# Kernel optimization log

Measured on AMD Instinct MI355X. Metric: run time of the kernel, lower is better.

The kernel has to match this reference:

```python
import jax, jax.numpy as jnp
import numpy as np


def setup_inputs() -> dict:
    key = jax.random.key(0)
    k1, k2, k3, k4 = jax.random.split(key, 4)
    B, S, H, U, C = 64, 512, 768, 16, 5
    hidden = jax.random.normal(k1, (B, S, H), dtype=jnp.float32)
    # per-token utterance index, sorted so each utterance is a contiguous span
    segment_ids = jnp.sort(jax.random.randint(k2, (B, S), 0, U), axis=-1).astype(jnp.int32)
    W_h = jax.random.normal(k3, (H, H), dtype=jnp.float32) * 0.02
    b_h = jnp.zeros((H,), dtype=jnp.float32)
    W_o = jax.random.normal(k4, (H, C), dtype=jnp.float32) * 0.02
    b_o = jnp.zeros((C,), dtype=jnp.float32)
    return {"hidden": hidden, "segment_ids": segment_ids, "n_utter": U,
            "W_h": W_h, "b_h": b_h, "W_o": W_o, "b_o": b_o}


def reference(hidden, segment_ids, n_utter, W_h, b_h, W_o, b_o):
    # hidden: [B,S,H]; segment_ids: [B,S] in [0, n_utter)
    B, S, H = hidden.shape
    n_segments = B * n_utter
    # globalize segment ids across the batch
    flat_seg = (segment_ids + jnp.arange(B, dtype=segment_ids.dtype)[:, None] * n_utter).reshape(-1)
    flat_h = hidden.reshape(B * S, H)
    # ragged per-utterance mean via one segment reduce (replaces python slice loop)
    sums = jax.ops.segment_sum(flat_h, flat_seg, num_segments=n_segments)
    counts = jax.ops.segment_sum(jnp.ones((B * S,), dtype=hidden.dtype), flat_seg,
                                 num_segments=n_segments)
    means = sums / jnp.maximum(counts, 1.0)[:, None]  # [B*n_utter, H]
    # linear_h -> SELU -> (dropout is identity in eval) -> linear_o -> softmax
    h = jax.nn.selu(means @ W_h + b_h)
    logits = h @ W_o + b_o
    return jax.nn.softmax(logits, axis=1)
```

## Files before the change

### kernel.cpp

```cpp
#include <hip/hip_runtime.h>
#include <math.h>

#define B 64
#define S 512
#define H 768
#define U 16
#define C 5
#define M (B*U)

typedef __attribute__((ext_vector_type(8))) short short8;
typedef __attribute__((ext_vector_type(4))) float floatx4;

__device__ inline unsigned short f2bf(float x) {
    unsigned u = __float_as_uint(x);
    u += 0x7FFFu + ((u >> 16) & 1u);
    return (unsigned short)(u >> 16);
}
__device__ inline float bf2f(unsigned short b) {
    return __uint_as_float((unsigned)b << 16);
}
__device__ inline void acc4(float4& a, const float4& v) {
    a.x += v.x; a.y += v.y; a.z += v.z; a.w += v.w;
}

__global__ __launch_bounds__(192) void prep_kernel(
    const float* __restrict__ hidden, const int* __restrict__ seg,
    const float* __restrict__ Wh,
    unsigned short* __restrict__ means, unsigned short* __restrict__ Bt)
{
    __shared__ float tile[32][33];
    const int t = threadIdx.x;

    if (blockIdx.x < M) {
        const int b = blockIdx.x >> 4;
        const int u = blockIdx.x & 15;
        const int* srow = seg + b * S;

        int lo = 0, hi = S;
        while (lo < hi) { int mid = (lo + hi) >> 1; if (srow[mid] < u) lo = mid + 1; else hi = mid; }
        const int start = lo;
        hi = S;
        while (lo < hi) { int mid = (lo + hi) >> 1; if (srow[mid] < u + 1) lo = mid + 1; else hi = mid; }
        const int end = lo;

        const float4* h4 = (const float4*)(hidden + (size_t)b * S * H) + t;
        const int ldr = H / 4;

        float4 a0 = make_float4(0.f,0.f,0.f,0.f), a1 = a0, a2 = a0, a3 = a0;
        int s = start;
        #pragma unroll 2
        for (; s + 4 <= end; s += 4) {
            float4 v0 = h4[(size_t)(s + 0) * ldr];
            float4 v1 = h4[(size_t)(s + 1) * ldr];
            float4 v2 = h4[(size_t)(s + 2) * ldr];
            float4 v3 = h4[(size_t)(s + 3) * ldr];
            acc4(a0, v0); acc4(a1, v1); acc4(a2, v2); acc4(a3, v3);
        }
        for (; s < end; ++s) acc4(a0, h4[(size_t)s * ldr]);

        acc4(a0, a1); acc4(a2, a3); acc4(a0, a2);
        const float inv = 1.0f / fmaxf((float)(end - start), 1.0f);
        ushort4 o;
        o.x = f2bf(a0.x * inv); o.y = f2bf(a0.y * inv);
        o.z = f2bf(a0.z * inv); o.w = f2bf(a0.w * inv);
        ((ushort4*)(means + (size_t)(b * U + u) * H))[t] = o;
        return;
    }

    const int tb = blockIdx.x - M;
    const int bn = tb % (H / 32);
    const int bk = tb / (H / 32);
    #pragma unroll
    for (int i = 0; i < 6; ++i) {
        int idx = t + 192 * i;
        if (idx < 1024) {
            int r = idx >> 5, c = idx & 31;
            tile[r][c] = Wh[(size_t)(bk * 32 + r) * H + bn * 32 + c];
        }
    }
    __syncthreads();
    #pragma unroll
    for (int i = 0; i < 6; ++i) {
        int idx = t + 192 * i;
        if (idx < 1024) {
            int r = idx >> 5, c = idx & 31;
            Bt[(size_t)(bn * 32 + r) * H + bk * 32 + c] = f2bf(tile[c][r]);
        }
    }
}

__global__ __launch_bounds__(256) void gemm1_mfma_kernel(
    const unsigned short* __restrict__ means, const unsigned short* __restrict__ Bt,
    const float* __restrict__ bh, unsigned short* __restrict__ hout)
{
    const int wid  = threadIdx.x >> 6;
    const int lane = threadIdx.x & 63;
    const int tile = blockIdx.x * 4 + wid;
    const int tm = tile / (H / 32);
    const int tn = tile % (H / 32);
    const int m0 = tm * 32, n0 = tn * 32;

    const int quad = lane >> 4;
    const int l16  = lane & 15;

    const short8* ap0 = (const short8*)(means + (size_t)(m0 + l16) * H);
    const short8* ap1 = (const short8*)(means + (size_t)(m0 + 16 + l16) * H);
    const short8* bp0 = (const short8*)(Bt    + (size_t)(n0 + l16) * H);
    const short8* bp1 = (const short8*)(Bt    + (size_t)(n0 + 16 + l16) * H);

    floatx4 acc00 = {0.f, 0.f, 0.f, 0.f}, acc01 = acc00, acc10 = acc00, acc11 = acc00;
    #pragma unroll 4
    for (int kk = 0; kk < H / 32; ++kk) {
        short8 a0 = ap0[4 * kk + quad];
        short8 a1 = ap1[4 * kk + quad];
        short8 b0 = bp0[4 * kk + quad];
        short8 b1 = bp1[4 * kk + quad];
        acc00 = __builtin_amdgcn_mfma_f32_16x16x32_bf16(a0, b0, acc00, 0, 0, 0);
        acc01 = __builtin_amdgcn_mfma_f32_16x16x32_bf16(a0, b1, acc01, 0, 0, 0);
        acc10 = __builtin_amdgcn_mfma_f32_16x16x32_bf16(a1, b0, acc10, 0, 0, 0);
        acc11 = __builtin_amdgcn_mfma_f32_16x16x32_bf16(a1, b1, acc11, 0, 0, 0);
    }

    const float SC = 1.0507009873554805f, AL = 1.6732632423543772f;
    const float bs0 = bh[n0 + l16], bs1 = bh[n0 + 16 + l16];
    #pragma unroll
    for (int r = 0; r < 4; ++r) {
        unsigned short* row0 = hout + (size_t)(m0 + quad * 4 + r) * H;
        unsigned short* row1 = hout + (size_t)(m0 + 16 + quad * 4 + r) * H;
        float x;
        x = acc00[r] + bs0; row0[n0 + l16]      = f2bf(x > 0.f ? SC * x : SC * AL * (expf(x) - 1.f));
        x = acc01[r] + bs1; row0[n0 + 16 + l16] = f2bf(x > 0.f ? SC * x : SC * AL * (expf(x) - 1.f));
        x = acc10[r] + bs0; row1[n0 + l16]      = f2bf(x > 0.f ? SC * x : SC * AL * (expf(x) - 1.f));
        x = acc11[r] + bs1; row1[n0 + 16 + l16] = f2bf(x > 0.f ? SC * x : SC * AL * (expf(x) - 1.f));
    }
}

__global__ __launch_bounds__(256) void head_kernel(
    const unsigned short* __restrict__ hbuf, const float* __restrict__ Wo,
    const float* __restrict__ bo, float* __restrict__ out)
{
    const int wave = threadIdx.x >> 6;
    const int lane = threadIdx.x & 63;
    const int row  = blockIdx.x * 4 + wave;

    float acc[C] = {};
    #pragma unroll
    for (int j = 0; j < H / 128; ++j) {
        int k = 128 * j + 2 * lane;
        ushort2 hv = *(const ushort2*)(hbuf + (size_t)row * H + k);
        float h0 = bf2f(hv.x), h1 = bf2f(hv.y);
        #pragma unroll
        for (int cc = 0; cc < C; ++cc)
            acc[cc] += h0 * Wo[(size_t)k * C + cc] + h1 * Wo[(size_t)(k + 1) * C + cc];
    }
    #pragma unroll
    for (int off = 32; off >= 1; off >>= 1)
        #pragma unroll
        for (int cc = 0; cc < C; ++cc) acc[cc] += __shfl_down(acc[cc], off);

    if (lane == 0) {
        float l[C], mx = -1e30f;
        #pragma unroll
        for (int cc = 0; cc < C; ++cc) { l[cc] = acc[cc] + bo[cc]; mx = fmaxf(mx, l[cc]); }
        float sum = 0.f;
        #pragma unroll
        for (int cc = 0; cc < C; ++cc) { l[cc] = expf(l[cc] - mx); sum += l[cc]; }
        float r = 1.0f / sum;
        #pragma unroll
        for (int cc = 0; cc < C; ++cc) out[(size_t)row * C + cc] = l[cc] * r;
    }
}

extern "C" void kernel_launch(void* const* d_in, const int* in_sizes, int n_in,
                              void* d_out, int out_size, void* d_ws, size_t ws_size,
                              hipStream_t stream)
{
    const float* hidden = (const float*)d_in[0];
    const int*   seg    = (const int*)d_in[1];
    const float* Wh = (const float*)d_in[3];
    const float* bh = (const float*)d_in[4];
    const float* Wo = (const float*)d_in[5];
    const float* bo = (const float*)d_in[6];
    float* out = (float*)d_out;

    unsigned short* means = (unsigned short*)d_ws;
    unsigned short* Bt    = means + (size_t)M * H;
    unsigned short* hbuf  = Bt + (size_t)H * H;

    prep_kernel<<<M + (H / 32) * (H / 32), 192, 0, stream>>>(hidden, seg, Wh, means, Bt);
    gemm1_mfma_kernel<<<(M / 32) * (H / 32) / 4, 256, 0, stream>>>(means, Bt, bh, hbuf);
    head_kernel<<<M / 4, 256, 0, stream>>>(hbuf, Wo, bo, out);
}
```

Measured before the change: 181.3 us.

## Fuse three kernels into one cooperative kernel with grid-wide syncs

Merges the segment-mean/weight-transpose prep, the MFMA GEMM with SELU, and the softmax head into a single cooperative kernel of M blocks separated by grid.sync calls. The aim is to remove two kernel launch gaps and inter-kernel drain. The cost is that the GEMM now runs at 3 waves per block over fewer active blocks, and the grid syncs add their own overhead. The launch also depends on all 1024 blocks being co-resident.

```diff
diff --git a/kernel.cpp b/kernel.cpp
--- a/kernel.cpp
+++ b/kernel.cpp
@@ -1,5 +1,8 @@
 #include <hip/hip_runtime.h>
+#include <hip/hip_cooperative_groups.h>
 #include <math.h>
+
+namespace cg = cooperative_groups;
 
 #define B 64
 #define S 512
@@ -23,17 +26,21 @@
     a.x += v.x; a.y += v.y; a.z += v.z; a.w += v.w;
 }
 
-__global__ __launch_bounds__(192) void prep_kernel(
+__global__ __launch_bounds__(192, 3) void fused_kernel(
     const float* __restrict__ hidden, const int* __restrict__ seg,
-    const float* __restrict__ Wh,
-    unsigned short* __restrict__ means, unsigned short* __restrict__ Bt)
+    const float* __restrict__ Wh, const float* __restrict__ bh,
+    const float* __restrict__ Wo, const float* __restrict__ bo,
+    unsigned short* __restrict__ means, unsigned short* __restrict__ Bt,
+    unsigned short* __restrict__ hbuf, float* __restrict__ out)
 {
+    cg::grid_group grid = cg::this_grid();
     __shared__ float tile[32][33];
-    const int t = threadIdx.x;
+    const int t  = threadIdx.x;
+    const int bi = blockIdx.x;
 
-    if (blockIdx.x < M) {
-        const int b = blockIdx.x >> 4;
-        const int u = blockIdx.x & 15;
+    {
+        const int b = bi >> 4;
+        const int u = bi & 15;
         const int* srow = seg + b * S;
 
         int lo = 0, hi = S;
@@ -63,111 +70,109 @@
         ushort4 o;
         o.x = f2bf(a0.x * inv); o.y = f2bf(a0.y * inv);
         o.z = f2bf(a0.z * inv); o.w = f2bf(a0.w * inv);
-        ((ushort4*)(means + (size_t)(b * U + u) * H))[t] = o;
-        return;
+        ((ushort4*)(means + (size_t)bi * H))[t] = o;
     }
 
-    const int tb = blockIdx.x - M;
-    const int bn = tb % (H / 32);
-    const int bk = tb / (H / 32);
-    #pragma unroll
-    for (int i = 0; i < 6; ++i) {
-        int idx = t + 192 * i;
-        if (idx < 1024) {
-            int r = idx >> 5, c = idx & 31;
-            tile[r][c] = Wh[(size_t)(bk * 32 + r) * H + bn * 32 + c];
+    if (bi < (H / 32) * (H / 32)) {
+        const int bn = bi % (H / 32);
+        const int bk = bi / (H / 32);
+        #pragma unroll
+        for (int i = 0; i < 6; ++i) {
+            int idx = t + 192 * i;
+            if (idx < 1024) {
+                int r = idx >> 5, c = idx & 31;
+                tile[r][c] = Wh[(size_t)(bk * 32 + r) * H + bn * 32 + c];
+            }
+        }
+        __syncthreads();
+        #pragma unroll
+        for (int i = 0; i < 6; ++i) {
+            int idx = t + 192 * i;
+            if (idx < 1024) {
+                int r = idx >> 5, c = idx & 31;
+                Bt[(size_t)(bn * 32 + r) * H + bk * 32 + c] = f2bf(tile[c][r]);
+            }
         }
     }
-    __syncthreads();
-    #pragma unroll
-    for (int i = 0; i < 6; ++i) {
-        int idx = t + 192 * i;
-        if (idx < 1024) {
-            int r = idx >> 5, c = idx & 31;
-            Bt[(size_t)(bn * 32 + r) * H + bk * 32 + c] = f2bf(tile[c][r]);
+
+    grid.sync();
+
+    const int wid  = t >> 6;
+    const int lane = t & 63;
+
+    if (bi < (M / 32) * (H / 32) / 3) {
+        const int tileId = bi * 3 + wid;
+        const int tm = tileId / (H / 32);
+        const int tn = tileId % (H / 32);
+        const int m0 = tm * 32, n0 = tn * 32;
+
+        const int quad = lane >> 4;
+        const int l16  = lane & 15;
+
+        const short8* ap0 = (const short8*)(means + (size_t)(m0 + l16) * H);
+        const short8* ap1 = (const short8*)(means + (size_t)(m0 + 16 + l16) * H);
+        const short8* bp0 = (const short8*)(Bt    + (size_t)(n0 + l16) * H);
+        const short8* bp1 = (const short8*)(Bt    + (size_t)(n0 + 16 + l16) * H);
+
+        floatx4 acc00 = {0.f, 0.f, 0.f, 0.f}, acc01 = acc00, acc10 = acc00, acc11 = acc00;
+        #pragma unroll 4
+        for (int kk = 0; kk < H / 32; ++kk) {
+            short8 a0 = ap0[4 * kk + quad];
+            short8 a1 = ap1[4 * kk + quad];
+            short8 b0 = bp0[4 * kk + quad];
+            short8 b1 = bp1[4 * kk + quad];
+            acc00 = __builtin_amdgcn_mfma_f32_16x16x32_bf16(a0, b0, acc00, 0, 0, 0);
+            acc01 = __builtin_amdgcn_mfma_f32_16x16x32_bf16(a0, b1, acc01, 0, 0, 0);
+            acc10 = __builtin_amdgcn_mfma_f32_16x16x32_bf16(a1, b0, acc10, 0, 0, 0);
+            acc11 = __builtin_amdgcn_mfma_f32_16x16x32_bf16(a1, b1, acc11, 0, 0, 0);
+        }
+
+        const float SC = 1.0507009873554805f, AL = 1.6732632423543772f;
+        const float bs0 = bh[n0 + l16], bs1 = bh[n0 + 16 + l16];
+        #pragma unroll
+        for (int r = 0; r < 4; ++r) {
+            unsigned short* row0 = hbuf + (size_t)(m0 + quad * 4 + r) * H;
+            unsigned short* row1 = hbuf + (size_t)(m0 + 16 + quad * 4 + r) * H;
+            float x;
+            x = acc00[r] + bs0; row0[n0 + l16]      = f2bf(x > 0.f ? SC * x : SC * AL * (expf(x) - 1.f));
+            x = acc01[r] + bs1; row0[n0 + 16 + l16] = f2bf(x > 0.f ? SC * x : SC * AL * (expf(x) - 1.f));
+            x = acc10[r] + bs0; row1[n0 + l16]      = f2bf(x > 0.f ? SC * x : SC * AL * (expf(x) - 1.f));
+            x = acc11[r] + bs1; row1[n0 + 16 + l16] = f2bf(x > 0.f ? SC * x : SC * AL * (expf(x) - 1.f));
         }
     }
-}
 
-__global__ __launch_bounds__(256) void gemm1_mfma_kernel(
-    const unsigned short* __restrict__ means, const unsigned short* __restrict__ Bt,
-    const float* __restrict__ bh, unsigned short* __restrict__ hout)
-{
-    const int wid  = threadIdx.x >> 6;
-    const int lane = threadIdx.x & 63;
-    const int tile = blockIdx.x * 4 + wid;
-    const int tm = tile / (H / 32);
-    const int tn = tile % (H / 32);
-    const int m0 = tm * 32, n0 = tn * 32;
+    grid.sync();
 
-    const int quad = lane >> 4;
-    const int l16  = lane & 15;
+    {
+        const int row = bi * 3 + wid;
+        if (row < M) {
+            float acc[C] = {};
+            #pragma unroll
+            for (int j = 0; j < H / 128; ++j) {
+                int k = 128 * j + 2 * lane;
+                ushort2 hv = *(const ushort2*)(hbuf + (size_t)row * H + k);
+                float h0 = bf2f(hv.x), h1 = bf2f(hv.y);
+                #pragma unroll
+                for (int cc = 0; cc < C; ++cc)
+                    acc[cc] += h0 * Wo[(size_t)k * C + cc] + h1 * Wo[(size_t)(k + 1) * C + cc];
+            }
+            #pragma unroll
+            for (int off = 32; off >= 1; off >>= 1)
+                #pragma unroll
+                for (int cc = 0; cc < C; ++cc) acc[cc] += __shfl_down(acc[cc], off);
 
-    const short8* ap0 = (const short8*)(means + (size_t)(m0 + l16) * H);
-    const short8* ap1 = (const short8*)(means + (size_t)(m0 + 16 + l16) * H);
-    const short8* bp0 = (const short8*)(Bt    + (size_t)(n0 + l16) * H);
-    const short8* bp1 = (const short8*)(Bt    + (size_t)(n0 + 16 + l16) * H);
-
-    floatx4 acc00 = {0.f, 0.f, 0.f, 0.f}, acc01 = acc00, acc10 = acc00, acc11 = acc00;
-    #pragma unroll 4
-    for (int kk = 0; kk < H / 32; ++kk) {
-        short8 a0 = ap0[4 * kk + quad];
-        short8 a1 = ap1[4 * kk + quad];
-        short8 b0 = bp0[4 * kk + quad];
-        short8 b1 = bp1[4 * kk + quad];
-        acc00 = __builtin_amdgcn_mfma_f32_16x16x32_bf16(a0, b0, acc00, 0, 0, 0);
-        acc01 = __builtin_amdgcn_mfma_f32_16x16x32_bf16(a0, b1, acc01, 0, 0, 0);
-        acc10 = __builtin_amdgcn_mfma_f32_16x16x32_bf16(a1, b0, acc10, 0, 0, 0);
-        acc11 = __builtin_amdgcn_mfma_f32_16x16x32_bf16(a1, b1, acc11, 0, 0, 0);
-    }
-
-    const float SC = 1.0507009873554805f, AL = 1.6732632423543772f;
-    const float bs0 = bh[n0 + l16], bs1 = bh[n0 + 16 + l16];
-    #pragma unroll
-    for (int r = 0; r < 4; ++r) {
-        unsigned short* row0 = hout + (size_t)(m0 + quad * 4 + r) * H;
-        unsigned short* row1 = hout + (size_t)(m0 + 16 + quad * 4 + r) * H;
-        float x;
-        x = acc00[r] + bs0; row0[n0 + l16]      = f2bf(x > 0.f ? SC * x : SC * AL * (expf(x) - 1.f));
-        x = acc01[r] + bs1; row0[n0 + 16 + l16] = f2bf(x > 0.f ? SC * x : SC * AL * (expf(x) - 1.f));
-        x = acc10[r] + bs0; row1[n0 + l16]      = f2bf(x > 0.f ? SC * x : SC * AL * (expf(x) - 1.f));
-        x = acc11[r] + bs1; row1[n0 + 16 + l16] = f2bf(x > 0.f ? SC * x : SC * AL * (expf(x) - 1.f));
-    }
-}
-
-__global__ __launch_bounds__(256) void head_kernel(
-    const unsigned short* __restrict__ hbuf, const float* __restrict__ Wo,
-    const float* __restrict__ bo, float* __restrict__ out)
-{
-    const int wave = threadIdx.x >> 6;
-    const int lane = threadIdx.x & 63;
-    const int row  = blockIdx.x * 4 + wave;
-
-    float acc[C] = {};
-    #pragma unroll
-    for (int j = 0; j < H / 128; ++j) {
-        int k = 128 * j + 2 * lane;
-        ushort2 hv = *(const ushort2*)(hbuf + (size_t)row * H + k);
-        float h0 = bf2f(hv.x), h1 = bf2f(hv.y);
-        #pragma unroll
-        for (int cc = 0; cc < C; ++cc)
-            acc[cc] += h0 * Wo[(size_t)k * C + cc] + h1 * Wo[(size_t)(k + 1) * C + cc];
-    }
-    #pragma unroll
-    for (int off = 32; off >= 1; off >>= 1)
-        #pragma unroll
-        for (int cc = 0; cc < C; ++cc) acc[cc] += __shfl_down(acc[cc], off);
-
-    if (lane == 0) {
-        float l[C], mx = -1e30f;
-        #pragma unroll
-        for (int cc = 0; cc < C; ++cc) { l[cc] = acc[cc] + bo[cc]; mx = fmaxf(mx, l[cc]); }
-        float sum = 0.f;
-        #pragma unroll
-        for (int cc = 0; cc < C; ++cc) { l[cc] = expf(l[cc] - mx); sum += l[cc]; }
-        float r = 1.0f / sum;
-        #pragma unroll
-        for (int cc = 0; cc < C; ++cc) out[(size_t)row * C + cc] = l[cc] * r;
+            if (lane == 0) {
+                float l[C], mx = -1e30f;
+                #pragma unroll
+                for (int cc = 0; cc < C; ++cc) { l[cc] = acc[cc] + bo[cc]; mx = fmaxf(mx, l[cc]); }
+                float sum = 0.f;
+                #pragma unroll
+                for (int cc = 0; cc < C; ++cc) { l[cc] = expf(l[cc] - mx); sum += l[cc]; }
+                float r = 1.0f / sum;
+                #pragma unroll
+                for (int cc = 0; cc < C; ++cc) out[(size_t)row * C + cc] = l[cc] * r;
+            }
+        }
     }
 }
 
@@ -187,7 +192,8 @@
     unsigned short* Bt    = means + (size_t)M * H;
     unsigned short* hbuf  = Bt + (size_t)H * H;
 
-    prep_kernel<<<M + (H / 32) * (H / 32), 192, 0, stream>>>(hidden, seg, Wh, means, Bt);
-    gemm1_mfma_kernel<<<(M / 32) * (H / 32) / 4, 256, 0, stream>>>(means, Bt, bh, hbuf);
-    head_kernel<<<M / 4, 256, 0, stream>>>(hbuf, Wo, bo, out);
+    void* args[] = { (void*)&hidden, (void*)&seg, (void*)&Wh, (void*)&bh,
+                     (void*)&Wo, (void*)&bo, (void*)&means, (void*)&Bt,
+                     (void*)&hbuf, (void*)&out };
+    hipLaunchCooperativeKernel((void*)fused_kernel, dim3(M), dim3(192), args, 0, stream);
 }
```

Result: slower. 434.2 us (+139.5%).

## Fuse hidden GEMM with output head using shared-memory row tiles

Applied to the files above, without the earlier changes.

Merges the bf16 MFMA GEMM and the softmax head into one kernel. Each 512-thread block computes a full 16-row strip of the hidden activations across all 768 columns and keeps it in LDS, then runs the 5-class projection and softmax from LDS. This removes one kernel launch and the global round-trip of the hidden buffer. In exchange it launches only 64 blocks, which lowers parallelism, and every block rereads all of Bt from global or L2 memory.

```diff
diff --git a/kernel.cpp b/kernel.cpp
--- a/kernel.cpp
+++ b/kernel.cpp
@@ -89,85 +89,83 @@
     }
 }
 
-__global__ __launch_bounds__(256) void gemm1_mfma_kernel(
+__global__ __launch_bounds__(512) void gemm_head_kernel(
     const unsigned short* __restrict__ means, const unsigned short* __restrict__ Bt,
-    const float* __restrict__ bh, unsigned short* __restrict__ hout)
+    const float* __restrict__ bh, const float* __restrict__ Wo,
+    const float* __restrict__ bo, float* __restrict__ out)
 {
+    __shared__ unsigned short hl[16][H + 4];
+
     const int wid  = threadIdx.x >> 6;
     const int lane = threadIdx.x & 63;
-    const int tile = blockIdx.x * 4 + wid;
-    const int tm = tile / (H / 32);
-    const int tn = tile % (H / 32);
-    const int m0 = tm * 32, n0 = tn * 32;
-
     const int quad = lane >> 4;
     const int l16  = lane & 15;
+    const int m0   = blockIdx.x * 16;
+    const int nb   = wid * 96;
 
-    const short8* ap0 = (const short8*)(means + (size_t)(m0 + l16) * H);
-    const short8* ap1 = (const short8*)(means + (size_t)(m0 + 16 + l16) * H);
-    const short8* bp0 = (const short8*)(Bt    + (size_t)(n0 + l16) * H);
-    const short8* bp1 = (const short8*)(Bt    + (size_t)(n0 + 16 + l16) * H);
+    const short8* ap = (const short8*)(means + (size_t)(m0 + l16) * H);
+    const short8* bp[6];
+    #pragma unroll
+    for (int tt = 0; tt < 6; ++tt)
+        bp[tt] = (const short8*)(Bt + (size_t)(nb + tt * 16 + l16) * H);
 
-    floatx4 acc00 = {0.f, 0.f, 0.f, 0.f}, acc01 = acc00, acc10 = acc00, acc11 = acc00;
-    #pragma unroll 4
+    floatx4 acc[6];
+    #pragma unroll
+    for (int tt = 0; tt < 6; ++tt) acc[tt] = (floatx4){0.f, 0.f, 0.f, 0.f};
+
+    #pragma unroll 2
     for (int kk = 0; kk < H / 32; ++kk) {
-        short8 a0 = ap0[4 * kk + quad];
-        short8 a1 = ap1[4 * kk + quad];
-        short8 b0 = bp0[4 * kk + quad];
-        short8 b1 = bp1[4 * kk + quad];
-        acc00 = __builtin_amdgcn_mfma_f32_16x16x32_bf16(a0, b0, acc00, 0, 0, 0);
-        acc01 = __builtin_amdgcn_mfma_f32_16x16x32_bf16(a0, b1, acc01, 0, 0, 0);
-        acc10 = __builtin_amdgcn_mfma_f32_16x16x32_bf16(a1, b0, acc10, 0, 0, 0);
-        acc11 = __builtin_amdgcn_mfma_f32_16x16x32_bf16(a1, b1, acc11, 0, 0, 0);
+        short8 a = ap[4 * kk + quad];
+        #pragma unroll
+        for (int tt = 0; tt < 6; ++tt) {
+            short8 b = bp[tt][4 * kk + quad];
+            acc[tt] = __builtin_amdgcn_mfma_f32_16x16x32_bf16(a, b, acc[tt], 0, 0, 0);
+        }
     }
 
     const float SC = 1.0507009873554805f, AL = 1.6732632423543772f;
-    const float bs0 = bh[n0 + l16], bs1 = bh[n0 + 16 + l16];
     #pragma unroll
-    for (int r = 0; r < 4; ++r) {
-        unsigned short* row0 = hout + (size_t)(m0 + quad * 4 + r) * H;
-        unsigned short* row1 = hout + (size_t)(m0 + 16 + quad * 4 + r) * H;
-        float x;
-        x = acc00[r] + bs0; row0[n0 + l16]      = f2bf(x > 0.f ? SC * x : SC * AL * (expf(x) - 1.f));
-        x = acc01[r] + bs1; row0[n0 + 16 + l16] = f2bf(x > 0.f ? SC * x : SC * AL * (expf(x) - 1.f));
-        x = acc10[r] + bs0; row1[n0 + l16]      = f2bf(x > 0.f ? SC * x : SC * AL * (expf(x) - 1.f));
-        x = acc11[r] + bs1; row1[n0 + 16 + l16] = f2bf(x > 0.f ? SC * x : SC * AL * (expf(x) - 1.f));
+    for (int tt = 0; tt < 6; ++tt) {
+        const float bs = bh[nb + tt * 16 + l16];
+        #pragma unroll
+        for (int r = 0; r < 4; ++r) {
+            float x = acc[tt][r] + bs;
+            hl[quad * 4 + r][nb + tt * 16 + l16] =
+                f2bf(x > 0.f ? SC * x : SC * AL * (expf(x) - 1.f));
+        }
     }
-}
 
-__global__ __launch_bounds__(256) void head_kernel(
-    const unsigned short* __restrict__ hbuf, const float* __restrict__ Wo,
-    const float* __restrict__ bo, float* __restrict__ out)
-{
-    const int wave = threadIdx.x >> 6;
-    const int lane = threadIdx.x & 63;
-    const int row  = blockIdx.x * 4 + wave;
+    __syncthreads();
 
-    float acc[C] = {};
     #pragma unroll
-    for (int j = 0; j < H / 128; ++j) {
-        int k = 128 * j + 2 * lane;
-        ushort2 hv = *(const ushort2*)(hbuf + (size_t)row * H + k);
-        float h0 = bf2f(hv.x), h1 = bf2f(hv.y);
+    for (int rr2 = 0; rr2 < 2; ++rr2) {
+        const int rr = wid * 2 + rr2;
+        float acc2[C] = {};
         #pragma unroll
-        for (int cc = 0; cc < C; ++cc)
-            acc[cc] += h0 * Wo[(size_t)k * C + cc] + h1 * Wo[(size_t)(k + 1) * C + cc];
-    }
-    #pragma unroll
-    for (int off = 32; off >= 1; off >>= 1)
+        for (int j = 0; j < H / 128; ++j) {
+            int k = 128 * j + 2 * lane;
+            ushort2 hv = *(const ushort2*)(&hl[rr][k]);
+            float h0 = bf2f(hv.x), h1 = bf2f(hv.y);
+            #pragma unroll
+            for (int cc = 0; cc < C; ++cc)
+                acc2[cc] += h0 * Wo[(size_t)k * C + cc] + h1 * Wo[(size_t)(k + 1) * C + cc];
+        }
         #pragma unroll
-        for (int cc = 0; cc < C; ++cc) acc[cc] += __shfl_down(acc[cc], off);
+        for (int off = 32; off >= 1; off >>= 1)
+            #pragma unroll
+            for (int cc = 0; cc < C; ++cc) acc2[cc] += __shfl_down(acc2[cc], off);
 
-    if (lane == 0) {
-        float l[C], mx = -1e30f;
-        #pragma unroll
-        for (int cc = 0; cc < C; ++cc) { l[cc] = acc[cc] + bo[cc]; mx = fmaxf(mx, l[cc]); }
-        float sum = 0.f;
-        #pragma unroll
-        for (int cc = 0; cc < C; ++cc) { l[cc] = expf(l[cc] - mx); sum += l[cc]; }
-        float r = 1.0f / sum;
-        #pragma unroll
-        for (int cc = 0; cc < C; ++cc) out[(size_t)row * C + cc] = l[cc] * r;
+        if (lane == 0) {
+            float l[C], mx = -1e30f;
+            #pragma unroll
+            for (int cc = 0; cc < C; ++cc) { l[cc] = acc2[cc] + bo[cc]; mx = fmaxf(mx, l[cc]); }
+            float sum = 0.f;
+            #pragma unroll
+            for (int cc = 0; cc < C; ++cc) { l[cc] = expf(l[cc] - mx); sum += l[cc]; }
+            float r = 1.0f / sum;
+            #pragma unroll
+            for (int cc = 0; cc < C; ++cc) out[(size_t)(m0 + rr) * C + cc] = l[cc] * r;
+        }
     }
 }
 
@@ -185,9 +183,7 @@
 
     unsigned short* means = (unsigned short*)d_ws;
     unsigned short* Bt    = means + (size_t)M * H;
-    unsigned short* hbuf  = Bt + (size_t)H * H;
 
     prep_kernel<<<M + (H / 32) * (H / 32), 192, 0, stream>>>(hidden, seg, Wh, means, Bt);
-    gemm1_mfma_kernel<<<(M / 32) * (H / 32) / 4, 256, 0, stream>>>(means, Bt, bh, hbuf);
-    head_kernel<<<M / 4, 256, 0, stream>>>(hbuf, Wo, bo, out);
+    gemm_head_kernel<<<M / 16, 512, 0, stream>>>(means, Bt, bh, Wo, bo, out);
 }
```

New measurement: 208.3 us. 1.15x slower.
